# Kernel tuning notes

Hardware: AMD Instinct MI355X
Metric: run time of the kernel (lower is better)

The kernel has to match this reference:

```python
import jax, jax.numpy as jnp
import numpy as np

H = 1024
NH = 16
HD = H // NH

def setup_inputs() -> dict:
    key = jax.random.key(0)
    ks = jax.random.split(key, 10)
    s = 1.0 / np.sqrt(H)
    return {
        "hiddenStates": jax.random.normal(ks[0], (2, 2048, H), dtype=jnp.float32),
        "attentionMask": jnp.zeros((2, 1, 1, 2048), dtype=jnp.float32),
        "Wq": jax.random.uniform(ks[1], (H, H), jnp.float32, -s, s),
        "bq": jax.random.uniform(ks[2], (H,), jnp.float32, -s, s),
        "Wk": jax.random.uniform(ks[3], (H, H), jnp.float32, -s, s),
        "bk": jax.random.uniform(ks[4], (H,), jnp.float32, -s, s),
        "Wv": jax.random.uniform(ks[5], (H, H), jnp.float32, -s, s),
        "bv": jax.random.uniform(ks[6], (H,), jnp.float32, -s, s),
        "Wo": jax.random.uniform(ks[7], (H, H), jnp.float32, -s, s),
        "bo": jax.random.uniform(ks[8], (H,), jnp.float32, -s, s),
    }

def _split_heads(x):
    # [B,S,H] -> [B,NH,S,HD]
    b, s, _ = x.shape
    return x.reshape(b, s, NH, HD).transpose(0, 2, 1, 3)

def reference(hiddenStates, attentionMask, Wq, bq, Wk, bk, Wv, bv, Wo, bo):
    q = _split_heads(hiddenStates @ Wq.T + bq)
    k = _split_heads(hiddenStates @ Wk.T + bk)
    v = _split_heads(hiddenStates @ Wv.T + bv)
    scores = jnp.einsum('bhqd,bhkd->bhqk', q, k) / np.sqrt(HD)
    scores = scores + attentionMask
    probs = jax.nn.softmax(scores, axis=-1)  # dropout p=0 -> identity
    ctx = jnp.einsum('bhqk,bhkd->bhqd', probs, v)
    b, _, s, _ = ctx.shape
    ctx = ctx.transpose(0, 2, 1, 3).reshape(b, s, H)
    return ctx @ Wo.T + bo
```

## Files before the change

### kernel.cpp

```cpp
#include <hip/hip_runtime.h>


#define BB   2
#define SS   2048
#define HH   1024
#define NHH  16
#define HDD  64

#define LOG2E 1.4426950408889634f
#define C1    (0.125f * LOG2E)

typedef _Float16 h8 __attribute__((ext_vector_type(8)));
typedef float f32x4 __attribute__((ext_vector_type(4)));
typedef float f32x16 __attribute__((ext_vector_type(16)));
typedef unsigned short us8 __attribute__((ext_vector_type(8)));
typedef unsigned u32x2 __attribute__((ext_vector_type(2)));

static __device__ __forceinline__ unsigned short f2h(float f) {
  return __builtin_bit_cast(unsigned short, (_Float16)f);
}
static __device__ __forceinline__ float h2f(unsigned short h) {
  return (float)__builtin_bit_cast(_Float16, h);
}
static __device__ __forceinline__ f32x4 mfma16(us8 a, us8 b, f32x4 c) {
  return __builtin_amdgcn_mfma_f32_16x16x32_f16(
      __builtin_bit_cast(h8, a), __builtin_bit_cast(h8, b), c, 0, 0, 0);
}
static __device__ __forceinline__ f32x16 mfma32(us8 a, us8 b, f32x16 c) {
  return __builtin_amdgcn_mfma_f32_32x32x16_f16(
      __builtin_bit_cast(h8, a), __builtin_bit_cast(h8, b), c, 0, 0, 0);
}
static __device__ __forceinline__ void gload16(const void* g, void* l) {
  __builtin_amdgcn_global_load_lds(
      (const __attribute__((address_space(1))) unsigned int*)g,
      (__attribute__((address_space(3))) unsigned int*)l, 16, 0, 0);
}
static __device__ __forceinline__ float exp2fast(float x) {
  float r; asm("v_exp_f32 %0, %1" : "=v"(r) : "v"(x)); return r;
}
static __device__ __forceinline__ unsigned cvtpkh(float lo, float hi) {
  unsigned r;
  asm("v_cvt_pkrtz_f16_f32 %0, %1, %2" : "=v"(r) : "v"(lo), "v"(hi));
  return r;
}
static __device__ __forceinline__ void pl32swap(unsigned& a, unsigned& b) {
  u32x2 r = __builtin_amdgcn_permlane32_swap(a, b, false, false);
  a = r[0]; b = r[1];
}
static __device__ __forceinline__ int fragoff(int lg, int r) {
  return (((lg << 10) + (r << 3)) ^ (lg << 3));
}
static __device__ __forceinline__ int fragoff0(int k, int hi) {
  return ((k >> 1) << 8) +
         (((((k & 1) << 7) | (hi << 4))) ^ (((k >> 1) & 7) << 4));
}

__global__ __launch_bounds__(256)
void pack_kernel(const float* __restrict__ X, const float* __restrict__ Wq,
                 const float* __restrict__ Wk, const float* __restrict__ Wv,
                 const float* __restrict__ Wo, const float* __restrict__ mask,
                 unsigned short* __restrict__ Xh,
                 unsigned short* __restrict__ Bh,
                 unsigned short* __restrict__ Oh,
                 float* __restrict__ maskl) {
  const int t = blockIdx.x;
  if (t == 2048) {
    const int i0 = threadIdx.x * 16;
#pragma unroll
    for (int j = 0; j < 4; ++j) {
      float4 v = *(const float4*)&mask[i0 + j * 4];
      v.x *= LOG2E; v.y *= LOG2E; v.z *= LOG2E; v.w *= LOG2E;
      *(float4*)&maskl[i0 + j * 4] = v;
    }
    return;
  }
  const float* src; unsigned short* dst;
  int smt, dmt, kt;
  if (t < 1024) { src = X; dst = Xh; smt = t >> 5; dmt = smt; kt = t & 31; }
  else {
    const int u = t - 1024, which = u >> 8, v = u & 255;
    smt = v >> 5; kt = v & 31;
    if (which == 0)      { src = Wq; dst = Bh; dmt = smt; }
    else if (which == 1) { src = Wk; dst = Bh; dmt = smt + 8; }
    else if (which == 2) { src = Wv; dst = Bh; dmt = smt + 16; }
    else                 { src = Wo; dst = Oh; dmt = smt; }
  }
  const size_t tb = ((size_t)(dmt * 32 + kt)) << 12;
#pragma unroll
  for (int it = 0; it < 2; ++it) {
    const int item = it * 256 + threadIdx.x;
    const int r = item >> 2, lg = item & 3;
    const float* sp = &src[(size_t)(smt * 128 + r) * HH + kt * 32 + lg * 8];
    const float4 a = *(const float4*)sp;
    const float4 b = *(const float4*)(sp + 4);
    const float vals[8] = {a.x, a.y, a.z, a.w, b.x, b.y, b.z, b.w};
    us8 h;
#pragma unroll
    for (int e = 0; e < 8; ++e) h[e] = f2h(vals[e]);
    *(us8*)&dst[tb + fragoff(lg, r)] = h;
  }
}

__global__ __launch_bounds__(256, 3)
void qkv_gemm_kernel(const unsigned short* __restrict__ Ah_,
                     const unsigned short* __restrict__ Bh_,
                     const float* __restrict__ bq, const float* __restrict__ bk,
                     const float* __restrict__ bv,
                     unsigned short* __restrict__ qb,
                     unsigned short* __restrict__ kb,
                     unsigned short* __restrict__ vt) {
  __shared__ __align__(16) unsigned short tiles[2][2][4096];
  const int tid = threadIdx.x, lane = tid & 63, wid = tid >> 6;
  const int l16 = lane & 15, lg = lane >> 4;
  const int wr = wid >> 1, wc = wid & 1;
  const int mt0 = blockIdx.y, nt0 = blockIdx.x;

  const unsigned short* gA = Ah_ + (((size_t)mt0 * 32) << 12);
  const unsigned short* gB = Bh_ + (((size_t)nt0 * 32) << 12);

#define GSTAGE(buf, kt_)                                                       \
  {                                                                            \
    const size_t ko_ = ((size_t)(kt_)) << 12;                                  \
    _Pragma("unroll")                                                          \
    for (int it_ = 0; it_ < 2; ++it_) {                                        \
      const int c_ = it_ * 256 + tid;                                          \
      gload16(gA + ko_ + c_ * 8, (char*)&tiles[buf][0][0] + c_ * 16);          \
      gload16(gB + ko_ + c_ * 8, (char*)&tiles[buf][1][0] + c_ * 16);          \
    }                                                                          \
  }

  f32x4 acc[4][4] = {};
  GSTAGE(0, 0)
  __syncthreads();
  for (int kt = 0; kt < 32; ++kt) {
    const int buf = kt & 1;
    if (kt + 1 < 32) GSTAGE(buf ^ 1, kt + 1)

    us8 a[4], b[4];
#pragma unroll
    for (int t = 0; t < 4; ++t) {
      a[t] = *(const us8*)&tiles[buf][0][fragoff(lg, wr * 64 + t * 16 + l16)];
      b[t] = *(const us8*)&tiles[buf][1][fragoff(lg, wc * 64 + t * 16 + l16)];
    }
#pragma unroll
    for (int mt = 0; mt < 4; ++mt)
#pragma unroll
      for (int nt = 0; nt < 4; ++nt)
        acc[mt][nt] = mfma16(a[mt], b[nt], acc[mt][nt]);
    __syncthreads();
  }
#undef GSTAGE

  const int m0 = mt0 * 128, n0 = nt0 * 128;
#pragma unroll
  for (int nt = 0; nt < 4; ++nt) {
    const int col = n0 + wc * 64 + nt * 16 + l16;
    const int which = col >> 10, nn = col & 1023;
    const float bias = (which == 0) ? bq[nn] : ((which == 1) ? bk[nn] : bv[nn]);
    const int h = nn >> 6, d = nn & 63;
#pragma unroll
    for (int mt = 0; mt < 4; ++mt) {
      const int row0 = m0 + wr * 64 + mt * 16 + lg * 4;
      const int bi = row0 >> 11, si0 = row0 & 2047;
      const size_t head = (size_t)(bi * NHH + h);
      if (which == 2) {
        ushort4 vv;
#pragma unroll
        for (int reg = 0; reg < 4; ++reg)
          ((unsigned short*)&vv)[reg] = f2h(acc[mt][nt][reg] + bias);
        *(ushort4*)&vt[(head * HDD + d) * SS + si0] = vv;
      } else {
#pragma unroll
        for (int reg = 0; reg < 4; ++reg) {
          const unsigned short v16 = f2h(acc[mt][nt][reg] + bias);
          if (which == 0) qb[(head * SS + si0 + reg) * HDD + d] = v16;
          else            kb[(head * SS + si0 + reg) * HDD + d] = v16;
        }
      }
    }
  }
}

__global__ __launch_bounds__(512)
void attn_kernel(const unsigned short* __restrict__ qb,
                 const unsigned short* __restrict__ kbuf,
                 const unsigned short* __restrict__ vt,
                 const float* __restrict__ maskl,
                 unsigned short* __restrict__ Op0,
                 unsigned short* __restrict__ Op1,
                 unsigned short* __restrict__ Op2,
                 unsigned short* __restrict__ Op3,
                 float* __restrict__ Ls) {
  __shared__ __align__(16) unsigned short Klds[2][4096];
  __shared__ __align__(16) unsigned short Vlds[2][4096];
  __shared__ __align__(16) float Msk[512];

  const int tid = threadIdx.x, lane = tid & 63, w = tid >> 6;
  const int q = lane & 31, hi = lane >> 5;
  const int bh = blockIdx.x;
  const int bi = bh >> 4, h = bh & 15;
  const int quarter = blockIdx.y >> 3;
  const int q0 = (blockIdx.y & 7) * 256 + w * 32;
  const int kbase = quarter * 512;
  const size_t bhS = (size_t)bh * SS;
  const int qrow = q0 + q;

  us8 qf[4];
#pragma unroll
  for (int ks = 0; ks < 4; ++ks)
    qf[ks] = *(const us8*)&qb[(bhS + qrow) * HDD + ks * 16 + hi * 8];

  const int koff0 = fragoff0(q, hi);
  const int koff1 = fragoff0(32 + q, hi);

  f32x16 o0 = {}, o1 = {};
  float lrun = 0.0f;

#define STAGE(buf, kt_)                                                        \
  {                                                                            \
    const int key0_ = kbase + (kt_) * 64;                                      \
    const int row_ = tid >> 4;                       \
    const int ss_ = (tid & 15) ^ (row_ & 7);                                   \
    const int kd_ = 2 * row_ + (ss_ >> 3);                                     \
    const int el_ = (ss_ & 7) * 8;                                             \
    gload16(&kbuf[(bhS + key0_ + kd_) * HDD + el_],                            \
            (char*)&Klds[buf][0] + tid * 16);                                  \
    gload16(&vt[((size_t)bh * HDD + kd_) * SS + key0_ + el_],                  \
            (char*)&Vlds[buf][0] + tid * 16);                                  \
  }

  if (w < 2)
    gload16(&maskl[bi * SS + kbase + tid * 4], (char*)&Msk[0] + tid * 16);
  STAGE(0, 0)
  __syncthreads();

  for (int kt = 0; kt < 8; ++kt) {
    const int buf = kt & 1;
    if (kt + 1 < 8) STAGE(buf ^ 1, kt + 1)
    const char* kb0 = (const char*)&Klds[0][0] + buf * 8192;
    const char* vb0 = (const char*)&Vlds[0][0] + buf * 8192;

    f32x16 s0 = {}, s1 = {};
    __builtin_amdgcn_s_setprio(1);
#pragma unroll
    for (int ks = 0; ks < 4; ++ks) {
      const us8 kf0 = *(const us8*)(kb0 + (koff0 ^ (ks << 5)));
      const us8 kf1 = *(const us8*)(kb0 + (koff1 ^ (ks << 5)));
      s0 = mfma32(kf0, qf[ks], s0);
      s1 = mfma32(kf1, qf[ks], s1);
    }
    __builtin_amdgcn_s_setprio(0);

#pragma unroll
    for (int g = 0; g < 4; ++g) {
      const float4 m0v = *(const float4*)&Msk[kt * 64 + g * 8 + hi * 4];
      const float4 m1v = *(const float4*)&Msk[kt * 64 + 32 + g * 8 + hi * 4];
      const float mm0[4] = {m0v.x, m0v.y, m0v.z, m0v.w};
      const float mm1[4] = {m1v.x, m1v.y, m1v.z, m1v.w};
#pragma unroll
      for (int j = 0; j < 4; ++j) {
        const int reg = g * 4 + j;
        s0[reg] = exp2fast(s0[reg] * C1 + mm0[j]);
        s1[reg] = exp2fast(s1[reg] * C1 + mm1[j]);
      }
    }
    float pa = 0.0f, pb_ = 0.0f, pc = 0.0f, pd = 0.0f;
#pragma unroll
    for (int g = 0; g < 4; ++g) {
      pa += s0[g * 4];     pb_ += s0[g * 4 + 1];
      pc += s0[g * 4 + 2]; pd += s0[g * 4 + 3];
      pa += s1[g * 4];     pb_ += s1[g * 4 + 1];
      pc += s1[g * 4 + 2]; pd += s1[g * 4 + 3];
    }
    float ps = (pa + pb_) + (pc + pd);
    ps += __shfl_xor(ps, 32);
    lrun += ps;

    us8 pb[4];
    {
      unsigned C[8];
#pragma unroll
      for (int j = 0; j < 8; ++j) C[j] = cvtpkh(s0[2 * j], s0[2 * j + 1]);
      pl32swap(C[0], C[2]); pl32swap(C[1], C[3]);
      pl32swap(C[4], C[6]); pl32swap(C[5], C[7]);
      union { unsigned wd[4]; us8 v; } u0, u1;
      u0.wd[0] = C[0]; u0.wd[1] = C[1]; u0.wd[2] = C[2]; u0.wd[3] = C[3];
      u1.wd[0] = C[4]; u1.wd[1] = C[5]; u1.wd[2] = C[6]; u1.wd[3] = C[7];
      pb[0] = u0.v; pb[1] = u1.v;
#pragma unroll
      for (int j = 0; j < 8; ++j) C[j] = cvtpkh(s1[2 * j], s1[2 * j + 1]);
      pl32swap(C[0], C[2]); pl32swap(C[1], C[3]);
      pl32swap(C[4], C[6]); pl32swap(C[5], C[7]);
      u0.wd[0] = C[0]; u0.wd[1] = C[1]; u0.wd[2] = C[2]; u0.wd[3] = C[3];
      u1.wd[0] = C[4]; u1.wd[1] = C[5]; u1.wd[2] = C[6]; u1.wd[3] = C[7];
      pb[2] = u0.v; pb[3] = u1.v;
    }

    __builtin_amdgcn_s_setprio(1);
#pragma unroll
    for (int ks = 0; ks < 4; ++ks) {
      const us8 vf0 = *(const us8*)(vb0 + (koff0 ^ (ks << 5)));
      const us8 vf1 = *(const us8*)(vb0 + (koff1 ^ (ks << 5)));
      o0 = mfma32(vf0, pb[ks], o0);
      o1 = mfma32(vf1, pb[ks], o1);
    }
    __builtin_amdgcn_s_setprio(0);

    __syncthreads();
  }

  unsigned short* opq = (quarter == 0) ? Op0 : (quarter == 1) ? Op1
                       : (quarter == 2) ? Op2 : Op3;
  unsigned short* op = opq + (bhS + qrow) * HDD;
#pragma unroll
  for (int g = 0; g < 4; ++g) {
    ushort4 v0, v1;
#pragma unroll
    for (int j = 0; j < 4; ++j) {
      ((unsigned short*)&v0)[j] = f2h(o0[g * 4 + j]);
      ((unsigned short*)&v1)[j] = f2h(o1[g * 4 + j]);
    }
    *(ushort4*)&op[g * 8 + hi * 4]      = v0;
    *(ushort4*)&op[32 + g * 8 + hi * 4] = v1;
  }
  if (hi == 0)
    Ls[((size_t)quarter * 32 + bh) * SS + qrow] = lrun;
#undef STAGE
}

__global__ __launch_bounds__(256)
void combine_kernel(const unsigned short* __restrict__ Op0,
                    const unsigned short* __restrict__ Op1,
                    const unsigned short* __restrict__ Op2,
                    const unsigned short* __restrict__ Op3,
                    const float* __restrict__ Ls,
                    unsigned short* __restrict__ Ch) {
  const int gid = blockIdx.x * 256 + threadIdx.x;
  const int row = gid >> 2, qtr = gid & 3;
  const int bh = row >> 11, s = row & 2047;
  const int bi = bh >> 4, h = bh & 15;

  const float tot = (Ls[row] + Ls[65536 + row]) +
                    (Ls[131072 + row] + Ls[196608 + row]);
  const float rinv = 1.0f / tot;

  const int d0 = qtr * 16;
  const us8* p0 = (const us8*)&Op0[(size_t)row * HDD + d0];
  const us8* p1 = (const us8*)&Op1[(size_t)row * HDD + d0];
  const us8* p2 = (const us8*)&Op2[(size_t)row * HDD + d0];
  const us8* p3 = (const us8*)&Op3[(size_t)row * HDD + d0];
  const us8 a0 = p0[0], a1 = p0[1];
  const us8 b0 = p1[0], b1 = p1[1];
  const us8 c0 = p2[0], c1 = p2[1];
  const us8 d0v = p3[0], d1 = p3[1];

  const int mrow = bi * SS + s;
  const int mt = mrow >> 7, r = mrow & 127;
#pragma unroll
  for (int j4 = 0; j4 < 4; ++j4) {
    const int col = h * 64 + d0 + j4 * 4;
    const int kt2 = col >> 5, lg2 = (col >> 3) & 3, e0 = col & 7;
    const size_t off = (((size_t)(mt * 32 + kt2)) << 12) + fragoff(lg2, r) + e0;
    ushort4 hv;
#pragma unroll
    for (int j = 0; j < 4; ++j) {
      const int k = j4 * 4 + j;
      const float va = h2f(k < 8 ? a0[k] : a1[k - 8]);
      const float vb = h2f(k < 8 ? b0[k] : b1[k - 8]);
      const float vc = h2f(k < 8 ? c0[k] : c1[k - 8]);
      const float vd = h2f(k < 8 ? d0v[k] : d1[k - 8]);
      ((unsigned short*)&hv)[j] = f2h(((va + vb) + (vc + vd)) * rinv);
    }
    *(ushort4*)&Ch[off] = hv;
  }
}

__global__ __launch_bounds__(256, 3)
void out_gemm_kernel(const unsigned short* __restrict__ Ah_,
                     const unsigned short* __restrict__ Bh_,
                     const float* __restrict__ bo, float* __restrict__ out) {
  __shared__ __align__(16) unsigned short tiles[2][2][4096];
  const int tid = threadIdx.x, lane = tid & 63, wid = tid >> 6;
  const int l16 = lane & 15, lg = lane >> 4;
  const int wr = wid >> 1, wc = wid & 1;
  const int mt0 = blockIdx.y, nt0 = blockIdx.x;

  const unsigned short* gA = Ah_ + (((size_t)mt0 * 32) << 12);
  const unsigned short* gB = Bh_ + (((size_t)nt0 * 32) << 12);

#define GSTAGE(buf, kt_)                                                       \
  {                                                                            \
    const size_t ko_ = ((size_t)(kt_)) << 12;                                  \
    _Pragma("unroll")                                                          \
    for (int it_ = 0; it_ < 2; ++it_) {                                        \
      const int c_ = it_ * 256 + tid;                                          \
      gload16(gA + ko_ + c_ * 8, (char*)&tiles[buf][0][0] + c_ * 16);          \
      gload16(gB + ko_ + c_ * 8, (char*)&tiles[buf][1][0] + c_ * 16);          \
    }                                                                          \
  }

  f32x4 acc[4][4] = {};
  GSTAGE(0, 0)
  __syncthreads();
  for (int kt = 0; kt < 32; ++kt) {
    const int buf = kt & 1;
    if (kt + 1 < 32) GSTAGE(buf ^ 1, kt + 1)

    us8 a[4], b[4];
#pragma unroll
    for (int t = 0; t < 4; ++t) {
      a[t] = *(const us8*)&tiles[buf][0][fragoff(lg, wr * 64 + t * 16 + l16)];
      b[t] = *(const us8*)&tiles[buf][1][fragoff(lg, wc * 64 + t * 16 + l16)];
    }
#pragma unroll
    for (int mt = 0; mt < 4; ++mt)
#pragma unroll
      for (int nt = 0; nt < 4; ++nt)
        acc[mt][nt] = mfma16(a[mt], b[nt], acc[mt][nt]);
    __syncthreads();
  }
#undef GSTAGE

  const int m0 = mt0 * 128, n0 = nt0 * 128;
#pragma unroll
  for (int nt = 0; nt < 4; ++nt) {
    const int col = n0 + wc * 64 + nt * 16 + l16;
    const float bias = bo[col];
#pragma unroll
    for (int mt = 0; mt < 4; ++mt)
#pragma unroll
      for (int reg = 0; reg < 4; ++reg) {
        const int row = m0 + wr * 64 + mt * 16 + lg * 4 + reg;
        out[(size_t)row * HH + col] = acc[mt][nt][reg] + bias;
      }
  }
}

extern "C" void kernel_launch(void* const* d_in, const int* in_sizes, int n_in,
                              void* d_out, int out_size, void* d_ws, size_t ws_size,
                              hipStream_t stream) {
  const float* X    = (const float*)d_in[0];
  const float* mask = (const float*)d_in[1];
  const float* Wq   = (const float*)d_in[2];
  const float* bq   = (const float*)d_in[3];
  const float* Wk   = (const float*)d_in[4];
  const float* bk   = (const float*)d_in[5];
  const float* Wv   = (const float*)d_in[6];
  const float* bv   = (const float*)d_in[7];
  const float* Wo   = (const float*)d_in[8];
  const float* bo   = (const float*)d_in[9];
  float* out = (float*)d_out;

  unsigned char* w = (unsigned char*)d_ws;
  const size_t MB = 1024 * 1024;
  unsigned short* Xh  = (unsigned short*)(w);
  unsigned short* Bh  = (unsigned short*)(w + 8 * MB);
  unsigned short* qb  = (unsigned short*)(w + 16 * MB);
  unsigned short* kb  = (unsigned short*)(w + 24 * MB);
  unsigned short* vt  = (unsigned short*)(w + 32 * MB);
  unsigned short* Op0 = (unsigned short*)(w + 40 * MB);
  unsigned short* Op1 = (unsigned short*)(w + 48 * MB);
  unsigned short* Op2 = Xh;
  unsigned short* Op3 = Bh;
  unsigned short* Oh  = (unsigned short*)(w + 56 * MB);
  float*          Ls  = (float*)(w + 58 * MB);
  float*       maskl  = (float*)(w + 59 * MB);
  unsigned short* Ch  = kb;

  pack_kernel<<<2049, 256, 0, stream>>>(X, Wq, Wk, Wv, Wo, mask,
                                        Xh, Bh, Oh, maskl);
  qkv_gemm_kernel<<<dim3(24, 32), 256, 0, stream>>>(Xh, Bh, bq, bk, bv,
                                                    qb, kb, vt);
  attn_kernel<<<dim3(32, 32), 512, 0, stream>>>(qb, kb, vt, maskl,
                                                Op0, Op1, Op2, Op3, Ls);
  combine_kernel<<<1024, 256, 0, stream>>>(Op0, Op1, Op2, Op3, Ls, Ch);
  out_gemm_kernel<<<dim3(8, 32), 256, 0, stream>>>(Ch, Oh, bo, out);
}
```

Measured before the change: 200.2 us.

## Process two 32-query tiles per wave in attention to reuse K/V fragments

Each wave now handles 64 query rows (two 32-row sub-tiles) instead of 32, so every K and V fragment read from LDS feeds two MFMAs. The grid's y-dimension is halved so each block covers 512 queries per key quarter. This cuts LDS reads and K/V staging traffic per unit of work. The cost is double the accumulator and score registers, which may lower occupancy, and half as many blocks, which may leave the GPU less evenly loaded.

```diff
diff --git a/kernel.cpp b/kernel.cpp
--- a/kernel.cpp
+++ b/kernel.cpp
@@ -199,22 +199,25 @@
   const int q = lane & 31, hi = lane >> 5;
   const int bh = blockIdx.x;
   const int bi = bh >> 4, h = bh & 15;
-  const int quarter = blockIdx.y >> 3;
-  const int q0 = (blockIdx.y & 7) * 256 + w * 32;
+  const int quarter = blockIdx.y >> 2;
+  const int q0 = (blockIdx.y & 3) * 512 + w * 64;
   const int kbase = quarter * 512;
   const size_t bhS = (size_t)bh * SS;
-  const int qrow = q0 + q;
-
-  us8 qf[4];
-#pragma unroll
-  for (int ks = 0; ks < 4; ++ks)
-    qf[ks] = *(const us8*)&qb[(bhS + qrow) * HDD + ks * 16 + hi * 8];
+  const int qrowA = q0 + q;
+  const int qrowB = q0 + 32 + q;
+
+  us8 qfA[4], qfB[4];
+#pragma unroll
+  for (int ks = 0; ks < 4; ++ks) {
+    qfA[ks] = *(const us8*)&qb[(bhS + qrowA) * HDD + ks * 16 + hi * 8];
+    qfB[ks] = *(const us8*)&qb[(bhS + qrowB) * HDD + ks * 16 + hi * 8];
+  }
 
   const int koff0 = fragoff0(q, hi);
   const int koff1 = fragoff0(32 + q, hi);
 
-  f32x16 o0 = {}, o1 = {};
-  float lrun = 0.0f;
+  f32x16 oA0 = {}, oA1 = {}, oB0 = {}, oB1 = {};
+  float lrunA = 0.0f, lrunB = 0.0f;
 
 #define STAGE(buf, kt_)                                                        \
   {                                                                            \
@@ -240,44 +243,53 @@
     const char* kb0 = (const char*)&Klds[0][0] + buf * 8192;
     const char* vb0 = (const char*)&Vlds[0][0] + buf * 8192;
 
-    f32x16 s0 = {}, s1 = {};
+    f32x16 sA0 = {}, sA1 = {}, sB0 = {}, sB1 = {};
     __builtin_amdgcn_s_setprio(1);
 #pragma unroll
     for (int ks = 0; ks < 4; ++ks) {
       const us8 kf0 = *(const us8*)(kb0 + (koff0 ^ (ks << 5)));
       const us8 kf1 = *(const us8*)(kb0 + (koff1 ^ (ks << 5)));
-      s0 = mfma32(kf0, qf[ks], s0);
-      s1 = mfma32(kf1, qf[ks], s1);
+      sA0 = mfma32(kf0, qfA[ks], sA0);
+      sB0 = mfma32(kf0, qfB[ks], sB0);
+      sA1 = mfma32(kf1, qfA[ks], sA1);
+      sB1 = mfma32(kf1, qfB[ks], sB1);
     }
     __builtin_amdgcn_s_setprio(0);
 
+    float mm0[16], mm1[16];
 #pragma unroll
     for (int g = 0; g < 4; ++g) {
       const float4 m0v = *(const float4*)&Msk[kt * 64 + g * 8 + hi * 4];
       const float4 m1v = *(const float4*)&Msk[kt * 64 + 32 + g * 8 + hi * 4];
-      const float mm0[4] = {m0v.x, m0v.y, m0v.z, m0v.w};
-      const float mm1[4] = {m1v.x, m1v.y, m1v.z, m1v.w};
-#pragma unroll
-      for (int j = 0; j < 4; ++j) {
-        const int reg = g * 4 + j;
-        s0[reg] = exp2fast(s0[reg] * C1 + mm0[j]);
-        s1[reg] = exp2fast(s1[reg] * C1 + mm1[j]);
+      mm0[g * 4 + 0] = m0v.x; mm0[g * 4 + 1] = m0v.y;
+      mm0[g * 4 + 2] = m0v.z; mm0[g * 4 + 3] = m0v.w;
+      mm1[g * 4 + 0] = m1v.x; mm1[g * 4 + 1] = m1v.y;
+      mm1[g * 4 + 2] = m1v.z; mm1[g * 4 + 3] = m1v.w;
+    }
+
+    us8 pbA[4], pbB[4];
+#pragma unroll
+    for (int half = 0; half < 2; ++half) {
+      f32x16& s0 = half ? sB0 : sA0;
+      f32x16& s1 = half ? sB1 : sA1;
+#pragma unroll
+      for (int r = 0; r < 16; ++r) {
+        s0[r] = exp2fast(s0[r] * C1 + mm0[r]);
+        s1[r] = exp2fast(s1[r] * C1 + mm1[r]);
       }
-    }
-    float pa = 0.0f, pb_ = 0.0f, pc = 0.0f, pd = 0.0f;
-#pragma unroll
-    for (int g = 0; g < 4; ++g) {
-      pa += s0[g * 4];     pb_ += s0[g * 4 + 1];
-      pc += s0[g * 4 + 2]; pd += s0[g * 4 + 3];
-      pa += s1[g * 4];     pb_ += s1[g * 4 + 1];
-      pc += s1[g * 4 + 2]; pd += s1[g * 4 + 3];
-    }
-    float ps = (pa + pb_) + (pc + pd);
-    ps += __shfl_xor(ps, 32);
-    lrun += ps;
-
-    us8 pb[4];
-    {
+      float pa = 0.0f, pb_ = 0.0f, pc = 0.0f, pd = 0.0f;
+#pragma unroll
+      for (int g = 0; g < 4; ++g) {
+        pa += s0[g * 4];     pb_ += s0[g * 4 + 1];
+        pc += s0[g * 4 + 2]; pd += s0[g * 4 + 3];
+        pa += s1[g * 4];     pb_ += s1[g * 4 + 1];
+        pc += s1[g * 4 + 2]; pd += s1[g * 4 + 3];
+      }
+      float ps = (pa + pb_) + (pc + pd);
+      ps += __shfl_xor(ps, 32);
+      if (half) lrunB += ps; else lrunA += ps;
+
+      us8* pb = half ? pbB : pbA;
       unsigned C[8];
 #pragma unroll
       for (int j = 0; j < 8; ++j) C[j] = cvtpkh(s0[2 * j], s0[2 * j + 1]);
@@ -301,8 +313,10 @@
     for (int ks = 0; ks < 4; ++ks) {
       const us8 vf0 = *(const us8*)(vb0 + (koff0 ^ (ks << 5)));
       const us8 vf1 = *(const us8*)(vb0 + (koff1 ^ (ks << 5)));
-      o0 = mfma32(vf0, pb[ks], o0);
-      o1 = mfma32(vf1, pb[ks], o1);
+      oA0 = mfma32(vf0, pbA[ks], oA0);
+      oB0 = mfma32(vf0, pbB[ks], oB0);
+      oA1 = mfma32(vf1, pbA[ks], oA1);
+      oB1 = mfma32(vf1, pbB[ks], oB1);
     }
     __builtin_amdgcn_s_setprio(0);
 
@@ -311,20 +325,26 @@
 
   unsigned short* opq = (quarter == 0) ? Op0 : (quarter == 1) ? Op1
                        : (quarter == 2) ? Op2 : Op3;
-  unsigned short* op = opq + (bhS + qrow) * HDD;
-#pragma unroll
-  for (int g = 0; g < 4; ++g) {
-    ushort4 v0, v1;
-#pragma unroll
-    for (int j = 0; j < 4; ++j) {
-      ((unsigned short*)&v0)[j] = f2h(o0[g * 4 + j]);
-      ((unsigned short*)&v1)[j] = f2h(o1[g * 4 + j]);
-    }
-    *(ushort4*)&op[g * 8 + hi * 4]      = v0;
-    *(ushort4*)&op[32 + g * 8 + hi * 4] = v1;
-  }
-  if (hi == 0)
-    Ls[((size_t)quarter * 32 + bh) * SS + qrow] = lrun;
+#pragma unroll
+  for (int half = 0; half < 2; ++half) {
+    const f32x16& o0 = half ? oB0 : oA0;
+    const f32x16& o1 = half ? oB1 : oA1;
+    const int qrow = half ? qrowB : qrowA;
+    unsigned short* op = opq + (bhS + qrow) * HDD;
+#pragma unroll
+    for (int g = 0; g < 4; ++g) {
+      ushort4 v0, v1;
+#pragma unroll
+      for (int j = 0; j < 4; ++j) {
+        ((unsigned short*)&v0)[j] = f2h(o0[g * 4 + j]);
+        ((unsigned short*)&v1)[j] = f2h(o1[g * 4 + j]);
+      }
+      *(ushort4*)&op[g * 8 + hi * 4]      = v0;
+      *(ushort4*)&op[32 + g * 8 + hi * 4] = v1;
+    }
+    if (hi == 0)
+      Ls[((size_t)quarter * 32 + bh) * SS + qrow] = half ? lrunB : lrunA;
+  }
 #undef STAGE
 }
 
@@ -471,7 +491,7 @@
                                         Xh, Bh, Oh, maskl);
   qkv_gemm_kernel<<<dim3(24, 32), 256, 0, stream>>>(Xh, Bh, bq, bk, bv,
                                                     qb, kb, vt);
-  attn_kernel<<<dim3(32, 32), 512, 0, stream>>>(qb, kb, vt, maskl,
+  attn_kernel<<<dim3(32, 16), 512, 0, stream>>>(qb, kb, vt, maskl,
                                                 Op0, Op1, Op2, Op3, Ls);
   combine_kernel<<<1024, 256, 0, stream>>>(Op0, Op1, Op2, Op3, Ls, Ch);
   out_gemm_kernel<<<dim3(8, 32), 256, 0, stream>>>(Ch, Oh, bo, out);
```

Result: no change. 202.2 us (+1.0%).
